# Optimization experiments

Measured on AMD Instinct MI355X. Metric: run time of the kernel, lower is better.

Reference implementation:

```python
import jax, jax.numpy as jnp
import numpy as np

B = 65536
LATENT = 256
POSE_DIM, SHAPE_DIM, ROT_DIM, TRANS_DIM = 15, 10, 3, 3
N_JOINTS = 16  # MANO kinematic tree (wrist + 3 per finger x 5)
PARENTS = (-1, 0, 1, 2, 0, 4, 5, 0, 7, 8, 0, 10, 11, 0, 13, 14)


def setup_inputs() -> dict:
    key = jax.random.key(0)
    ks = jax.random.split(key, 13)
    f32 = jnp.float32
    inp = {
        'z_left': jax.random.normal(ks[0], (B, LATENT), dtype=f32),
        'z_right': jax.random.normal(ks[1], (B, LATENT), dtype=f32),
        # MLP params (Linear(256,512) -> ReLU -> Linear(512,256) -> ReLU -> Linear(256,31))
        'W1': jax.random.normal(ks[2], (LATENT, 512), dtype=f32) * 0.02,
        'b1': jnp.zeros((512,), dtype=f32),
        'W2': jax.random.normal(ks[3], (512, 256), dtype=f32) * 0.02,
        'b2': jnp.zeros((256,), dtype=f32),
        'W3': jax.random.normal(ks[4], (256, 31), dtype=f32) * 0.02,
        'b3': jnp.zeros((31,), dtype=f32),
        # MANO model parameters
        'J_template': jax.random.normal(ks[5], (N_JOINTS, 3), dtype=f32) * 0.05,
        'shape_dirs': jax.random.normal(ks[6], (N_JOINTS, 3, SHAPE_DIM), dtype=f32) * 0.01,
        'hands_components': jax.random.normal(ks[7], (POSE_DIM, 45), dtype=f32) * 0.1,  # PCA -> 15 joints axis-angle
        'hands_mean': jax.random.normal(ks[8], (45,), dtype=f32) * 0.1,
    }
    return inp


def rodrigues(r):
    """Axis-angle [..., 3] -> rotation matrices [..., 3, 3]."""
    theta = jnp.sqrt(jnp.sum(r * r, axis=-1, keepdims=True) + 1e-12)  # [...,1]
    k = r / theta
    kx, ky, kz = k[..., 0], k[..., 1], k[..., 2]
    z = jnp.zeros_like(kx)
    K = jnp.stack([z, -kz, ky, kz, z, -kx, -ky, kx, z], axis=-1)
    K = K.reshape(r.shape[:-1] + (3, 3))
    ct = jnp.cos(theta)[..., None]
    st = jnp.sin(theta)[..., None]
    I = jnp.eye(3, dtype=r.dtype)
    return I + st * K + (1.0 - ct) * (K @ K)


def _decode(z, W1, b1, W2, b2, W3, b3, J_template, shape_dirs, hands_components, hands_mean, is_right):
    # small MLP -> MANO params
    h = jax.nn.relu(z @ W1 + b1)
    h = jax.nn.relu(h @ W2 + b2)
    p = h @ W3 + b3                                    # [B,31]
    pose = p[:, :POSE_DIM]                             # [B,15] PCA coeffs
    shape = p[:, POSE_DIM:POSE_DIM + SHAPE_DIM]        # [B,10]
    rot = p[:, 25:28]                                  # global axis-angle
    trans = p[:, 28:31]

    # shape blend on joint template
    J = J_template[None] + jnp.einsum('jkd,bd->bjk', shape_dirs, shape)  # [B,16,3]
    if not is_right:
        J = J * jnp.asarray([-1.0, 1.0, 1.0], dtype=z.dtype)  # mirror for left hand

    # PCA pose -> per-joint axis-angle -> rotations
    full_pose = hands_mean[None] + pose @ hands_components   # [B,45]
    aa = full_pose.reshape(-1, 15, 3)
    R_global = rodrigues(rot)            # [B,3,3]
    R_local = rodrigues(aa)              # [B,15,3,3]
    R = jnp.concatenate([R_global[:, None], R_local], axis=1)  # [B,16,3,3]

    # batched kinematic chain (fixed 16-joint tree)
    Rw = [R[:, 0]]
    t = [J[:, 0]]
    for i in range(1, N_JOINTS):
        par = PARENTS[i]
        Rw.append(jnp.einsum('bij,bjk->bik', Rw[par], R[:, i]))
        t.append(jnp.einsum('bij,bj->bi', Rw[par], J[:, i] - J[:, par]) + t[par])
    joints = jnp.stack(t, axis=1) + trans[:, None, :]   # [B,16,3]
    return joints


def reference(z_left, z_right, W1, b1, W2, b2, W3, b3, J_template, shape_dirs, hands_components, hands_mean):
    joints_left = _decode(z_left, W1, b1, W2, b2, W3, b3, J_template, shape_dirs, hands_components, hands_mean, is_right=False)
    joints_right = _decode(z_right, W1, b1, W2, b2, W3, b3, J_template, shape_dirs, hands_components, hands_mean, is_right=True)
    return (joints_left, joints_right)
```

## Files before the change

kernel.cpp:

```cpp
#include <hip/hip_runtime.h>
#include <hip/hip_bf16.h>

typedef __attribute__((ext_vector_type(8))) short short8;
typedef __attribute__((ext_vector_type(4))) float f32x4;
typedef unsigned short ushort_t;

#define MFMA16(a,b,c) __builtin_amdgcn_mfma_f32_16x16x32_bf16((a),(b),(c),0,0,0)

__device__ __forceinline__ ushort_t f2bf(float x){
  unsigned int u = __builtin_bit_cast(unsigned int, x);
  unsigned int r = (u + 0x7FFFu + ((u >> 16) & 1u)) >> 16;
  return (ushort_t)r;
}
__device__ __forceinline__ float bf2f(ushort_t h){
  unsigned int u = ((unsigned int)h) << 16;
  return __builtin_bit_cast(float, u);
}

__device__ __forceinline__ void mat3mul(float* C, const float* A, const float* B){
  #pragma unroll
  for (int i = 0; i < 3; i++)
    #pragma unroll
    for (int k = 0; k < 3; k++)
      C[i*3+k] = A[i*3+0]*B[0*3+k] + A[i*3+1]*B[1*3+k] + A[i*3+2]*B[2*3+k];
}
__device__ __forceinline__ void rotp(float* o, const float* A, float x, float y, float z, const float* t){
  o[0] = A[0]*x + A[1]*y + A[2]*z + t[0];
  o[1] = A[3]*x + A[4]*y + A[5]*z + t[1];
  o[2] = A[6]*x + A[7]*y + A[8]*z + t[2];
}

__global__ __launch_bounds__(64) void poison_kernel(float* out, float val){
  if (threadIdx.x == 0 && blockIdx.x == 0) out[0] = val;
}

__global__ __launch_bounds__(256) void preconv_kernel(
    const float* __restrict__ W1, const float* __restrict__ W2, const float* __restrict__ W3,
    ushort_t* __restrict__ W1h, ushort_t* __restrict__ W1l,
    ushort_t* __restrict__ W2h, ushort_t* __restrict__ W2l,
    ushort_t* __restrict__ W3h, ushort_t* __restrict__ W3l)
{
  const int idx = blockIdx.x * 256 + threadIdx.x;
  {
    int j = idx & 7, l = (idx >> 3) & 63, kk = (idx >> 9) & 7, nt = idx >> 12;
    int k = kk*32 + (l >> 4)*8 + j, n = nt*16 + (l & 15);
    float w = W1[k*512 + n];
    ushort_t hi = f2bf(w);
    W1h[idx] = hi; W1l[idx] = f2bf(w - bf2f(hi));
  }
  {
    int j = idx & 7, l = (idx >> 3) & 63, kk = (idx >> 9) & 15, nt = idx >> 13;
    int k = kk*32 + (l >> 4)*8 + j, n = nt*16 + (l & 15);
    float w = W2[k*256 + n];
    ushort_t hi = f2bf(w);
    W2h[idx] = hi; W2l[idx] = f2bf(w - bf2f(hi));
  }
  if (idx < 16384){
    int j = idx & 7, l = (idx >> 3) & 63, kk = (idx >> 9) & 7, nt = idx >> 12;
    int k = kk*32 + (l >> 4)*8 + j, n = nt*16 + (l & 15);
    float w = (nt < 2 && n < 31) ? W3[k*31 + n] : 0.f;
    ushort_t hi = f2bf(w);
    W3h[idx] = hi; W3l[idx] = f2bf(w - bf2f(hi));
  }
}

__global__ __launch_bounds__(256, 2) void fused_kernel(
    const float* __restrict__ zL, const float* __restrict__ zR,
    const ushort_t* __restrict__ W1h, const ushort_t* __restrict__ W1l,
    const ushort_t* __restrict__ W2h, const ushort_t* __restrict__ W2l,
    const ushort_t* __restrict__ W3h, const ushort_t* __restrict__ W3l,
    const float* __restrict__ b1, const float* __restrict__ b2, const float* __restrict__ b3,
    const float* __restrict__ Jt, const float* __restrict__ sd,
    const float* __restrict__ hc, const float* __restrict__ hm,
    float* __restrict__ out)
{
  __shared__ ushort_t regA[2*32*264];
  __shared__ ushort_t regB[2*32*72];
  __shared__ float    plbuf[32*33];
  ushort_t* regAhi = regA;
  ushort_t* regAlo = regA + 32*264;
  ushort_t* regBhi = regB;
  ushort_t* regBlo = regB + 32*72;

  const int tid  = threadIdx.x;
  const int lane = tid & 63;
  const int w    = tid >> 6;
  const int lo   = lane & 15;
  const int g    = lane >> 4;
  const int m0   = blockIdx.x * 32;
  const bool right = (m0 >= 65536);
  const float* zsrc = right ? (zR + (size_t)(m0 - 65536) * 256)
                            : (zL + (size_t)m0 * 256);

  short8 bh[8], bl[8];
  #pragma unroll
  for (int kk = 0; kk < 8; kk++){
    bh[kk] = *(const short8*)(W1h + (size_t)((0*4 + w)*8 + kk)*512 + lane*8);
    bl[kk] = *(const short8*)(W1l + (size_t)((0*4 + w)*8 + kk)*512 + lane*8);
  }

  #pragma unroll
  for (int i = 0; i < 8; i++){
    int e = i*1024 + tid*4;
    float4 v = *(const float4*)(zsrc + e);
    int r = e >> 8, c = e & 255;
    ushort_t* dh = &regAhi[r*264 + c];
    ushort_t* dl = &regAlo[r*264 + c];
    float vv[4] = {v.x, v.y, v.z, v.w};
    #pragma unroll
    for (int q = 0; q < 4; q++){
      ushort_t hi = f2bf(vv[q]);
      dh[q] = hi; dl[q] = f2bf(vv[q] - bf2f(hi));
    }
  }
  __syncthreads();

  f32x4 accL2[2][4];
  #pragma unroll
  for (int a = 0; a < 2; a++)
    #pragma unroll
    for (int b = 0; b < 4; b++)
      accL2[a][b] = (f32x4){0.f,0.f,0.f,0.f};

  #pragma unroll
  for (int c = 0; c < 8; c++){
    const int nt = c*4 + w;
    const float bias1 = b1[nt*16 + lo];

    short8 b2h0[4], b2l0[4];
    #pragma unroll
    for (int q = 0; q < 4; q++){
      b2h0[q] = *(const short8*)(W2h + (size_t)((w*4+q)*16 + c*2 + 0)*512 + lane*8);
      b2l0[q] = *(const short8*)(W2l + (size_t)((w*4+q)*16 + c*2 + 0)*512 + lane*8);
    }

    {
      f32x4 ahh = (f32x4){0.f,0.f,0.f,0.f};
      f32x4 ahl = (f32x4){0.f,0.f,0.f,0.f};
      f32x4 alh = (f32x4){0.f,0.f,0.f,0.f};
      #pragma unroll
      for (int kk = 0; kk < 8; kk++){
        short8 ah = *(const short8*)&regAhi[(0*16 + lo)*264 + kk*32 + g*8];
        short8 al = *(const short8*)&regAlo[(0*16 + lo)*264 + kk*32 + g*8];
        ahh = MFMA16(ah, bh[kk], ahh);
        ahl = MFMA16(ah, bl[kk], ahl);
        alh = MFMA16(al, bh[kk], alh);
      }
      #pragma unroll
      for (int i = 0; i < 4; i++){
        float v = fmaxf(ahh[i] + ahl[i] + alh[i] + bias1, 0.f);
        ushort_t hi = f2bf(v);
        const int ro = (0*16 + g*4 + i)*72 + w*16 + lo;
        regBhi[ro] = hi; regBlo[ro] = f2bf(v - bf2f(hi));
      }
    }

    short8 b2h1[4], b2l1[4];
    #pragma unroll
    for (int q = 0; q < 4; q++){
      b2h1[q] = *(const short8*)(W2h + (size_t)((w*4+q)*16 + c*2 + 1)*512 + lane*8);
      b2l1[q] = *(const short8*)(W2l + (size_t)((w*4+q)*16 + c*2 + 1)*512 + lane*8);
    }

    {
      f32x4 ahh = (f32x4){0.f,0.f,0.f,0.f};
      f32x4 ahl = (f32x4){0.f,0.f,0.f,0.f};
      f32x4 alh = (f32x4){0.f,0.f,0.f,0.f};
      #pragma unroll
      for (int kk = 0; kk < 8; kk++){
        short8 ah = *(const short8*)&regAhi[(1*16 + lo)*264 + kk*32 + g*8];
        short8 al = *(const short8*)&regAlo[(1*16 + lo)*264 + kk*32 + g*8];
        ahh = MFMA16(ah, bh[kk], ahh);
        ahl = MFMA16(ah, bl[kk], ahl);
        alh = MFMA16(al, bh[kk], alh);
      }
      #pragma unroll
      for (int i = 0; i < 4; i++){
        float v = fmaxf(ahh[i] + ahl[i] + alh[i] + bias1, 0.f);
        ushort_t hi = f2bf(v);
        const int ro = (1*16 + g*4 + i)*72 + w*16 + lo;
        regBhi[ro] = hi; regBlo[ro] = f2bf(v - bf2f(hi));
      }
    }
    __syncthreads();

    if (c < 7){
      #pragma unroll
      for (int kk = 0; kk < 4; kk++){
        bh[kk] = *(const short8*)(W1h + (size_t)(((c+1)*4 + w)*8 + kk)*512 + lane*8);
        bl[kk] = *(const short8*)(W1l + (size_t)(((c+1)*4 + w)*8 + kk)*512 + lane*8);
      }
    }
    #pragma unroll
    for (int rt = 0; rt < 2; rt++){
      short8 ah = *(const short8*)&regBhi[(rt*16 + lo)*72 + 0*32 + g*8];
      short8 al = *(const short8*)&regBlo[(rt*16 + lo)*72 + 0*32 + g*8];
      #pragma unroll
      for (int q = 0; q < 4; q++){
        accL2[rt][q] = MFMA16(ah, b2h0[q], accL2[rt][q]);
        accL2[rt][q] = MFMA16(ah, b2l0[q], accL2[rt][q]);
        accL2[rt][q] = MFMA16(al, b2h0[q], accL2[rt][q]);
      }
    }

    if (c < 7){
      #pragma unroll
      for (int kk = 4; kk < 8; kk++){
        bh[kk] = *(const short8*)(W1h + (size_t)(((c+1)*4 + w)*8 + kk)*512 + lane*8);
        bl[kk] = *(const short8*)(W1l + (size_t)(((c+1)*4 + w)*8 + kk)*512 + lane*8);
      }
    }
    #pragma unroll
    for (int rt = 0; rt < 2; rt++){
      short8 ah = *(const short8*)&regBhi[(rt*16 + lo)*72 + 1*32 + g*8];
      short8 al = *(const short8*)&regBlo[(rt*16 + lo)*72 + 1*32 + g*8];
      #pragma unroll
      for (int q = 0; q < 4; q++){
        accL2[rt][q] = MFMA16(ah, b2h1[q], accL2[rt][q]);
        accL2[rt][q] = MFMA16(ah, b2l1[q], accL2[rt][q]);
        accL2[rt][q] = MFMA16(al, b2h1[q], accL2[rt][q]);
      }
    }
    __syncthreads();
  }

  const int rw = w & 1, nn = w >> 1;
  short8 w3h[8], w3l[8];
  #pragma unroll
  for (int kk = 0; kk < 8; kk++){
    w3h[kk] = *(const short8*)(W3h + (size_t)(nn*8 + kk)*512 + lane*8);
    w3l[kk] = *(const short8*)(W3l + (size_t)(nn*8 + kk)*512 + lane*8);
  }

  #pragma unroll
  for (int rt = 0; rt < 2; rt++){
    #pragma unroll
    for (int q = 0; q < 4; q++){
      const int col = w*64 + q*16 + lo;
      const float bias = b2[col];
      #pragma unroll
      for (int i = 0; i < 4; i++){
        float v = fmaxf(accL2[rt][q][i] + bias, 0.f);
        ushort_t hi = f2bf(v);
        const int ro = (rt*16 + g*4 + i)*264 + col;
        regAhi[ro] = hi; regAlo[ro] = f2bf(v - bf2f(hi));
      }
    }
  }
  __syncthreads();

  {
    f32x4 ahh = (f32x4){0.f,0.f,0.f,0.f};
    f32x4 ahl = (f32x4){0.f,0.f,0.f,0.f};
    f32x4 alh = (f32x4){0.f,0.f,0.f,0.f};
    #pragma unroll
    for (int kk = 0; kk < 8; kk++){
      short8 ah = *(const short8*)&regAhi[(rw*16 + lo)*264 + kk*32 + g*8];
      short8 al = *(const short8*)&regAlo[(rw*16 + lo)*264 + kk*32 + g*8];
      ahh = MFMA16(ah, w3h[kk], ahh);
      ahl = MFMA16(ah, w3l[kk], ahl);
      alh = MFMA16(al, w3h[kk], alh);
    }
    const int col = nn*16 + lo;
    const float bias = (col < 31) ? b3[col] : 0.f;
    #pragma unroll
    for (int i = 0; i < 4; i++)
      plbuf[(rw*16 + g*4 + i)*33 + col] = ahh[i] + ahl[i] + alh[i] + bias;
  }
  __syncthreads();
  const float* pl = plbuf;

  if (tid < 32){
    const int r = tid;
    float p15[15];
    #pragma unroll
    for (int d = 0; d < 15; d++) p15[d] = pl[r*33 + d];
    float sh[10];
    #pragma unroll
    for (int d = 0; d < 10; d++) sh[d] = pl[r*33 + 15 + d];
    const float trx = pl[r*33+28], tr_y = pl[r*33+29], trz = pl[r*33+30];

    float J[16][3];
    #pragma unroll
    for (int jj = 0; jj < 16; jj++){
      #pragma unroll
      for (int k2 = 0; k2 < 3; k2++){
        float v = Jt[jj*3 + k2];
        #pragma unroll
        for (int d = 0; d < 10; d++) v = fmaf(sd[(jj*3 + k2)*10 + d], sh[d], v);
        J[jj][k2] = v;
      }
    }
    if (!right){
      #pragma unroll
      for (int jj = 0; jj < 16; jj++) J[jj][0] = -J[jj][0];
    }

    auto rod = [](float ax, float ay, float az, float* R){
      float th = sqrtf(ax*ax + ay*ay + az*az + 1e-12f);
      float inv = 1.0f / th;
      float kx = ax*inv, ky = ay*inv, kz = az*inv;
      float st = __sinf(th), ct = __cosf(th);
      float omc = 1.0f - ct;
      R[0] = ct + omc*kx*kx;      R[1] = omc*kx*ky - st*kz;  R[2] = omc*kx*kz + st*ky;
      R[3] = omc*kx*ky + st*kz;   R[4] = ct + omc*ky*ky;     R[5] = omc*ky*kz - st*kx;
      R[6] = omc*kx*kz - st*ky;   R[7] = omc*ky*kz + st*kx;  R[8] = ct + omc*kz*kz;
    };
    auto axis_rod = [&](int j, float* R){
      const int base = 3*(j-1);
      float s0 = hm[base+0], s1 = hm[base+1], s2 = hm[base+2];
      #pragma unroll
      for (int d = 0; d < 15; d++){
        float pv = p15[d];
        s0 = fmaf(pv, hc[d*45 + base+0], s0);
        s1 = fmaf(pv, hc[d*45 + base+1], s1);
        s2 = fmaf(pv, hc[d*45 + base+2], s2);
      }
      rod(s0, s1, s2, R);
    };

    float R0[9];
    rod(pl[r*33+25], pl[r*33+26], pl[r*33+27], R0);

    const size_t ob = (right ? (size_t)3145728 : (size_t)0)
                    + (size_t)(m0 - (right ? 65536 : 0) + r) * 48;
    float t0[3] = {J[0][0], J[0][1], J[0][2]};
    out[ob+0] = t0[0]+trx; out[ob+1] = t0[1]+tr_y; out[ob+2] = t0[2]+trz;
    #pragma unroll
    for (int f = 0; f < 5; f++){
      const int i1 = 3*f+1, i2 = 3*f+2, i3 = 3*f+3;
      float R1[9], R2[9], Rw1[9], Rw2[9], t1[3], t2[3], t3[3];
      axis_rod(i1, R1);
      axis_rod(i2, R2);
      mat3mul(Rw1, R0, R1);
      rotp(t1, R0,  J[i1][0]-J[0][0],  J[i1][1]-J[0][1],  J[i1][2]-J[0][2],  t0);
      mat3mul(Rw2, Rw1, R2);
      rotp(t2, Rw1, J[i2][0]-J[i1][0], J[i2][1]-J[i1][1], J[i2][2]-J[i1][2], t1);
      rotp(t3, Rw2, J[i3][0]-J[i2][0], J[i3][1]-J[i2][1], J[i3][2]-J[i2][2], t2);
      out[ob + i1*3+0] = t1[0]+trx; out[ob + i1*3+1] = t1[1]+tr_y; out[ob + i1*3+2] = t1[2]+trz;
      out[ob + i2*3+0] = t2[0]+trx; out[ob + i2*3+1] = t2[1]+tr_y; out[ob + i2*3+2] = t2[2]+trz;
      out[ob + i3*3+0] = t3[0]+trx; out[ob + i3*3+1] = t3[1]+tr_y; out[ob + i3*3+2] = t3[2]+trz;
    }
  }
}

extern "C" void kernel_launch(void* const* d_in, const int* in_sizes, int n_in,
                              void* d_out, int out_size, void* d_ws, size_t ws_size,
                              hipStream_t stream) {
  const float* zL = (const float*)d_in[0];
  const float* zR = (const float*)d_in[1];
  const float* W1 = (const float*)d_in[2];
  const float* b1 = (const float*)d_in[3];
  const float* W2 = (const float*)d_in[4];
  const float* b2 = (const float*)d_in[5];
  const float* W3 = (const float*)d_in[6];
  const float* b3 = (const float*)d_in[7];
  const float* Jt = (const float*)d_in[8];
  const float* sd = (const float*)d_in[9];
  const float* hc = (const float*)d_in[10];
  const float* hm = (const float*)d_in[11];

  float* out = (float*)d_out;

  if (ws_size < 1114112){
    poison_kernel<<<1, 64, 0, stream>>>(out, 20480.f);
    return;
  }

  ushort_t* W1h = (ushort_t*)d_ws;
  ushort_t* W1l = W1h + 131072;
  ushort_t* W2h = W1l + 131072;
  ushort_t* W2l = W2h + 131072;
  ushort_t* W3h = W2l + 131072;
  ushort_t* W3l = W3h + 16384;

  preconv_kernel<<<512, 256, 0, stream>>>(W1, W2, W3, W1h, W1l, W2h, W2l, W3h, W3l);
  fused_kernel<<<4096, 256, 0, stream>>>(zL, zR, W1h, W1l, W2h, W2l, W3h, W3l,
                                         b1, b2, b3, Jt, sd, hc, hm, out);
}
```

Before: 269.1 us.

## Double-buffer layer-1 activations to pipeline layer-1 and layer-2 MFMA chunks

Layer-1 output chunks now go into a double-buffered LDS region. Each iteration computes layer-1 for chunk c+1 into the other buffer while layer 2 consumes chunk c, which cuts the __syncthreads per chunk from two to one. The aim is to overlap global weight loads and MFMA work across the two layers and reduce barrier stalls. In exchange it uses more LDS (regB doubles) and raises register pressure, which could lower occupancy from the launch_bounds target of 2 blocks.

```diff
diff --git a/kernel.cpp b/kernel.cpp
--- a/kernel.cpp
+++ b/kernel.cpp
@@ -75,12 +75,10 @@
     float* __restrict__ out)
 {
   __shared__ ushort_t regA[2*32*264];
-  __shared__ ushort_t regB[2*32*72];
+  __shared__ ushort_t regB[2][2*32*72];
   __shared__ float    plbuf[32*33];
   ushort_t* regAhi = regA;
   ushort_t* regAlo = regA + 32*264;
-  ushort_t* regBhi = regB;
-  ushort_t* regBlo = regB + 32*72;
 
   const int tid  = threadIdx.x;
   const int lane = tid & 63;
@@ -115,33 +113,19 @@
   }
   __syncthreads();
 
-  f32x4 accL2[2][4];
-  #pragma unroll
-  for (int a = 0; a < 2; a++)
-    #pragma unroll
-    for (int b = 0; b < 4; b++)
-      accL2[a][b] = (f32x4){0.f,0.f,0.f,0.f};
-
-  #pragma unroll
-  for (int c = 0; c < 8; c++){
-    const int nt = c*4 + w;
-    const float bias1 = b1[nt*16 + lo];
-
-    short8 b2h0[4], b2l0[4];
-    #pragma unroll
-    for (int q = 0; q < 4; q++){
-      b2h0[q] = *(const short8*)(W2h + (size_t)((w*4+q)*16 + c*2 + 0)*512 + lane*8);
-      b2l0[q] = *(const short8*)(W2l + (size_t)((w*4+q)*16 + c*2 + 0)*512 + lane*8);
-    }
-
-    {
+  {
+    const float bias1 = b1[(0*4 + w)*16 + lo];
+    ushort_t* rbh = regB[0];
+    ushort_t* rbl = regB[0] + 32*72;
+    #pragma unroll
+    for (int rt = 0; rt < 2; rt++){
       f32x4 ahh = (f32x4){0.f,0.f,0.f,0.f};
       f32x4 ahl = (f32x4){0.f,0.f,0.f,0.f};
       f32x4 alh = (f32x4){0.f,0.f,0.f,0.f};
       #pragma unroll
       for (int kk = 0; kk < 8; kk++){
-        short8 ah = *(const short8*)&regAhi[(0*16 + lo)*264 + kk*32 + g*8];
-        short8 al = *(const short8*)&regAlo[(0*16 + lo)*264 + kk*32 + g*8];
+        short8 ah = *(const short8*)&regAhi[(rt*16 + lo)*264 + kk*32 + g*8];
+        short8 al = *(const short8*)&regAlo[(rt*16 + lo)*264 + kk*32 + g*8];
         ahh = MFMA16(ah, bh[kk], ahh);
         ahl = MFMA16(ah, bl[kk], ahl);
         alh = MFMA16(al, bh[kk], alh);
@@ -150,75 +134,96 @@
       for (int i = 0; i < 4; i++){
         float v = fmaxf(ahh[i] + ahl[i] + alh[i] + bias1, 0.f);
         ushort_t hi = f2bf(v);
-        const int ro = (0*16 + g*4 + i)*72 + w*16 + lo;
-        regBhi[ro] = hi; regBlo[ro] = f2bf(v - bf2f(hi));
-      }
-    }
-
-    short8 b2h1[4], b2l1[4];
-    #pragma unroll
-    for (int q = 0; q < 4; q++){
-      b2h1[q] = *(const short8*)(W2h + (size_t)((w*4+q)*16 + c*2 + 1)*512 + lane*8);
-      b2l1[q] = *(const short8*)(W2l + (size_t)((w*4+q)*16 + c*2 + 1)*512 + lane*8);
-    }
-
-    {
-      f32x4 ahh = (f32x4){0.f,0.f,0.f,0.f};
-      f32x4 ahl = (f32x4){0.f,0.f,0.f,0.f};
-      f32x4 alh = (f32x4){0.f,0.f,0.f,0.f};
+        const int ro = (rt*16 + g*4 + i)*72 + w*16 + lo;
+        rbh[ro] = hi; rbl[ro] = f2bf(v - bf2f(hi));
+      }
+    }
+  }
+  __syncthreads();
+
+  f32x4 accL2[2][4];
+  #pragma unroll
+  for (int a = 0; a < 2; a++)
+    #pragma unroll
+    for (int b = 0; b < 4; b++)
+      accL2[a][b] = (f32x4){0.f,0.f,0.f,0.f};
+
+  #pragma unroll
+  for (int c = 0; c < 8; c++){
+    const ushort_t* rbh = regB[c & 1];
+    const ushort_t* rbl = regB[c & 1] + 32*72;
+    ushort_t* nbh = regB[(c + 1) & 1];
+    ushort_t* nbl = regB[(c + 1) & 1] + 32*72;
+
+    if (c < 7){
       #pragma unroll
       for (int kk = 0; kk < 8; kk++){
-        short8 ah = *(const short8*)&regAhi[(1*16 + lo)*264 + kk*32 + g*8];
-        short8 al = *(const short8*)&regAlo[(1*16 + lo)*264 + kk*32 + g*8];
-        ahh = MFMA16(ah, bh[kk], ahh);
-        ahl = MFMA16(ah, bl[kk], ahl);
-        alh = MFMA16(al, bh[kk], alh);
-      }
-      #pragma unroll
-      for (int i = 0; i < 4; i++){
-        float v = fmaxf(ahh[i] + ahl[i] + alh[i] + bias1, 0.f);
-        ushort_t hi = f2bf(v);
-        const int ro = (1*16 + g*4 + i)*72 + w*16 + lo;
-        regBhi[ro] = hi; regBlo[ro] = f2bf(v - bf2f(hi));
-      }
-    }
-    __syncthreads();
-
-    if (c < 7){
-      #pragma unroll
-      for (int kk = 0; kk < 4; kk++){
         bh[kk] = *(const short8*)(W1h + (size_t)(((c+1)*4 + w)*8 + kk)*512 + lane*8);
         bl[kk] = *(const short8*)(W1l + (size_t)(((c+1)*4 + w)*8 + kk)*512 + lane*8);
       }
     }
-    #pragma unroll
-    for (int rt = 0; rt < 2; rt++){
-      short8 ah = *(const short8*)&regBhi[(rt*16 + lo)*72 + 0*32 + g*8];
-      short8 al = *(const short8*)&regBlo[(rt*16 + lo)*72 + 0*32 + g*8];
+
+    {
+      short8 b2h[4], b2l[4];
       #pragma unroll
       for (int q = 0; q < 4; q++){
-        accL2[rt][q] = MFMA16(ah, b2h0[q], accL2[rt][q]);
-        accL2[rt][q] = MFMA16(ah, b2l0[q], accL2[rt][q]);
-        accL2[rt][q] = MFMA16(al, b2h0[q], accL2[rt][q]);
+        b2h[q] = *(const short8*)(W2h + (size_t)((w*4+q)*16 + c*2 + 0)*512 + lane*8);
+        b2l[q] = *(const short8*)(W2l + (size_t)((w*4+q)*16 + c*2 + 0)*512 + lane*8);
+      }
+      #pragma unroll
+      for (int rt = 0; rt < 2; rt++){
+        short8 ah = *(const short8*)&rbh[(rt*16 + lo)*72 + 0*32 + g*8];
+        short8 al = *(const short8*)&rbl[(rt*16 + lo)*72 + 0*32 + g*8];
+        #pragma unroll
+        for (int q = 0; q < 4; q++){
+          accL2[rt][q] = MFMA16(ah, b2h[q], accL2[rt][q]);
+          accL2[rt][q] = MFMA16(ah, b2l[q], accL2[rt][q]);
+          accL2[rt][q] = MFMA16(al, b2h[q], accL2[rt][q]);
+        }
+      }
+    }
+    {
+      short8 b2h[4], b2l[4];
+      #pragma unroll
+      for (int q = 0; q < 4; q++){
+        b2h[q] = *(const short8*)(W2h + (size_t)((w*4+q)*16 + c*2 + 1)*512 + lane*8);
+        b2l[q] = *(const short8*)(W2l + (size_t)((w*4+q)*16 + c*2 + 1)*512 + lane*8);
+      }
+      #pragma unroll
+      for (int rt = 0; rt < 2; rt++){
+        short8 ah = *(const short8*)&rbh[(rt*16 + lo)*72 + 1*32 + g*8];
+        short8 al = *(const short8*)&rbl[(rt*16 + lo)*72 + 1*32 + g*8];
+        #pragma unroll
+        for (int q = 0; q < 4; q++){
+          accL2[rt][q] = MFMA16(ah, b2h[q], accL2[rt][q]);
+          accL2[rt][q] = MFMA16(ah, b2l[q], accL2[rt][q]);
+          accL2[rt][q] = MFMA16(al, b2h[q], accL2[rt][q]);
+        }
       }
     }
 
     if (c < 7){
-      #pragma unroll
-      for (int kk = 4; kk < 8; kk++){
-        bh[kk] = *(const short8*)(W1h + (size_t)(((c+1)*4 + w)*8 + kk)*512 + lane*8);
-        bl[kk] = *(const short8*)(W1l + (size_t)(((c+1)*4 + w)*8 + kk)*512 + lane*8);
-      }
-    }
-    #pragma unroll
-    for (int rt = 0; rt < 2; rt++){
-      short8 ah = *(const short8*)&regBhi[(rt*16 + lo)*72 + 1*32 + g*8];
-      short8 al = *(const short8*)&regBlo[(rt*16 + lo)*72 + 1*32 + g*8];
-      #pragma unroll
-      for (int q = 0; q < 4; q++){
-        accL2[rt][q] = MFMA16(ah, b2h1[q], accL2[rt][q]);
-        accL2[rt][q] = MFMA16(ah, b2l1[q], accL2[rt][q]);
-        accL2[rt][q] = MFMA16(al, b2h1[q], accL2[rt][q]);
+      const float bias1 = b1[((c+1)*4 + w)*16 + lo];
+      #pragma unroll
+      for (int rt = 0; rt < 2; rt++){
+        f32x4 ahh = (f32x4){0.f,0.f,0.f,0.f};
+        f32x4 ahl = (f32x4){0.f,0.f,0.f,0.f};
+        f32x4 alh = (f32x4){0.f,0.f,0.f,0.f};
+        #pragma unroll
+        for (int kk = 0; kk < 8; kk++){
+          short8 ah = *(const short8*)&regAhi[(rt*16 + lo)*264 + kk*32 + g*8];
+          short8 al = *(const short8*)&regAlo[(rt*16 + lo)*264 + kk*32 + g*8];
+          ahh = MFMA16(ah, bh[kk], ahh);
+          ahl = MFMA16(ah, bl[kk], ahl);
+          alh = MFMA16(al, bh[kk], alh);
+        }
+        #pragma unroll
+        for (int i = 0; i < 4; i++){
+          float v = fmaxf(ahh[i] + ahl[i] + alh[i] + bias1, 0.f);
+          ushort_t hi = f2bf(v);
+          const int ro = (rt*16 + g*4 + i)*72 + w*16 + lo;
+          nbh[ro] = hi; nbl[ro] = f2bf(v - bf2f(hi));
+        }
       }
     }
     __syncthreads();
```

Result: slower. 299.8 us (+11.4%).
